# Kernel tuning notes

Measured on AMD Instinct MI355X. Metric: run time of the kernel, lower is better.

Reference implementation:

```python
import jax, jax.numpy as jnp
import numpy as np

T, S, B = 128, 128, 32          # enc len, dec len, batch
H, D = 512, 512                 # hidden == input_size (required by module)
VE, VD = 32000, 32000           # encoder / decoder vocab


def setup_inputs() -> dict:
    key = jax.random.key(0)
    ks = jax.random.split(key, 14)
    s = 0.05  # init scale, mimics uniform(-initrange, initrange)
    n = lambda k, shape: jax.random.normal(k, shape, dtype=jnp.float32) * s
    return {
        "encoder_inputs": jax.random.randint(ks[0], (T, B), 0, VE),
        "decoder_inputs": jax.random.randint(ks[1], (S, B), 0, VD),
        "enc_emb": n(ks[2], (VE, D)),
        "dec_emb": n(ks[3], (VD, D)),
        "enc_Wih": n(ks[4], (4 * H, D)),   # torch LSTM gate order: i,f,g,o
        "enc_Whh": n(ks[5], (4 * H, H)),
        "dec_Wih": n(ks[6], (4 * H, H)),
        "dec_Whh": n(ks[7], (4 * H, H)),
        "attn_enc_W": n(ks[8], (H, H)),
        "attn_enc_b": n(ks[9], (H,)),
        "attn_dec_W": n(ks[10], (H, H)),
        "attn_dec_b": n(ks[11], (H,)),
        "out_W": n(ks[12], (VD, H)),
        "out_b": n(ks[13], (VD,)),
    }


def lstm(x, Wih, Whh, h0, c0):
    """Bias-free LSTM over seq-first x [T,B,Din]; returns (ys [T,B,H], (h,c))."""
    def step(carry, xt):
        h, c = carry
        gates = xt @ Wih.T + h @ Whh.T
        i, f, g, o = jnp.split(gates, 4, axis=-1)
        c = jax.nn.sigmoid(f) * c + jax.nn.sigmoid(i) * jnp.tanh(g)
        h = jax.nn.sigmoid(o) * jnp.tanh(c)
        return (h, c), h
    (h, c), ys = jax.lax.scan(step, (h0, c0), x)
    return ys, (h, c)


def reference(encoder_inputs, decoder_inputs, enc_emb, dec_emb,
              enc_Wih, enc_Whh, dec_Wih, dec_Whh,
              attn_enc_W, attn_enc_b, attn_dec_W, attn_dec_b,
              out_W, out_b):
    Bsz = encoder_inputs.shape[1]
    Hd = enc_Whh.shape[1]
    z = jnp.zeros((Bsz, Hd), dtype=enc_Whh.dtype)
    # encoder
    xe = enc_emb[encoder_inputs]                      # [T,B,D]
    enc_out, (h, c) = lstm(xe, enc_Wih, enc_Whh, z, z)
    # decoder (teacher forcing), init from encoder final state
    xd = dec_emb[decoder_inputs]                      # [S,B,H]
    dec_out, _ = lstm(xd, dec_Wih, dec_Whh, h, c)     # [S,B,H]
    # per-timestep dot attention, vectorized over all decoder steps
    scores = jnp.einsum('tbh,sbh->sbt', enc_out, dec_out)   # [S,B,T]
    attn = jax.nn.softmax(scores, axis=-1)
    ctx = jnp.einsum('sbt,tbh->sbh', attn, enc_out)          # [S,B,H]
    hidden = jnp.tanh(ctx @ attn_enc_W.T + attn_enc_b
                      + dec_out @ attn_dec_W.T + attn_dec_b)
    logits = hidden @ out_W.T + out_b                        # [S,B,VD]
    return jax.nn.log_softmax(logits, axis=-1)
```

## Files before the change

kernel.cpp:

```cpp
#include <hip/hip_runtime.h>
#include <stdint.h>

#define TT 128
#define BB 32
#define HH 512
#define MM 4096
#define VD 32000
#define NLB 16

typedef float f32x4 __attribute__((ext_vector_type(4)));
typedef short s16x8 __attribute__((ext_vector_type(8)));
typedef unsigned long long u64;

#define TAGMASK 0x0001000100010001ull

__device__ __forceinline__ ushort f2bf(float f){
  uint u = __float_as_uint(f);
  return (ushort)((u + 0x7fffu + ((u >> 16) & 1u)) >> 16);
}
__device__ __forceinline__ float bfl(uint v){ return __uint_as_float(v << 16); }
__device__ __forceinline__ float bfh(uint v){ return __uint_as_float(v & 0xffff0000u); }
__device__ __forceinline__ float bfu(ushort v){ return __uint_as_float(((uint)v) << 16); }
__device__ __forceinline__ float fast_tanh(float x){
  return 1.f - 2.f / (1.f + __expf(2.f * x));
}

__global__ void k_init(u64* hbuf){
  int i = blockIdx.x * 256 + threadIdx.x;
  if (i < 4096) hbuf[i] = 0ull;
  else if (i < 8192) hbuf[i] = TAGMASK;
}

__global__ __launch_bounds__(256) void k_cvt(const float* __restrict__ s, ushort* __restrict__ d, int n4){
  int i = blockIdx.x * 256 + threadIdx.x;
  int st = gridDim.x * 256;
  for (; i < n4; i += st){
    f32x4 v = *(const f32x4*)(s + (size_t)i * 4);
    ushort4 o; o.x = f2bf(v[0]); o.y = f2bf(v[1]); o.z = f2bf(v[2]); o.w = f2bf(v[3]);
    *(ushort4*)(d + (size_t)i * 4) = o;
  }
}

__global__ __launch_bounds__(128) void k_embed(const int* __restrict__ ids, const float* __restrict__ emb,
                                               ushort* __restrict__ out){
  int row = blockIdx.x, t = threadIdx.x;
  int id = ids[row];
  f32x4 v = *(const f32x4*)(emb + (size_t)id * HH + t * 4);
  ushort4 o; o.x = f2bf(v[0]); o.y = f2bf(v[1]); o.z = f2bf(v[2]); o.w = f2bf(v[3]);
  *(ushort4*)(out + (size_t)row * HH + t * 4) = o;
}

__global__ __launch_bounds__(128) void k_concatB(const float* __restrict__ We, const float* __restrict__ Wd,
                                                 ushort* __restrict__ Bc){
  int n = blockIdx.x, t = threadIdx.x;
  f32x4 a = *(const f32x4*)(We + (size_t)n * HH + t * 4);
  f32x4 b = *(const f32x4*)(Wd + (size_t)n * HH + t * 4);
  ushort4 oa, ob;
  oa.x = f2bf(a[0]); oa.y = f2bf(a[1]); oa.z = f2bf(a[2]); oa.w = f2bf(a[3]);
  ob.x = f2bf(b[0]); ob.y = f2bf(b[1]); ob.z = f2bf(b[2]); ob.w = f2bf(b[3]);
  *(ushort4*)(Bc + (size_t)n * 1024 + t * 4) = oa;
  *(ushort4*)(Bc + (size_t)n * 1024 + 512 + t * 4) = ob;
}
__global__ void k_bsum(const float* a, const float* b, float* o){
  int i = blockIdx.x * 256 + threadIdx.x;
  if (i < HH) o[i] = a[i] + b[i];
}

template<bool BIAS, bool TANH, bool OUTBF, bool LSE>
__global__ __launch_bounds__(256) void k_gemm(const ushort* __restrict__ A, const ushort* __restrict__ Bm,
                                              const float* __restrict__ bias, void* __restrict__ Cout,
                                              int Mtot, int Ntot, int K,
                                              float* __restrict__ pbufM, float* __restrict__ pbufL){
  __shared__ __align__(16) ushort As[128 * 32];
  __shared__ __align__(16) ushort Bs[128 * 32];
  __shared__ float sMm[2][128], sMl[2][128];
  const int tid = threadIdx.x;
  const int m0 = blockIdx.y << 7, n0 = blockIdx.x << 7;
  const int wid = tid >> 6, lane = tid & 63;
  const int wm = wid >> 1, wn = wid & 1;
  const int lr = lane & 15, lg = lane >> 4;
  const int lk = lg << 3, cr = lg << 2;
  f32x4 acc[4][4];
  for (int i = 0; i < 4; ++i)
    for (int j = 0; j < 4; ++j)
      acc[i][j] = (f32x4){0.f, 0.f, 0.f, 0.f};
  const int c0 = tid, c1 = tid + 256;
  const size_t ar0 = (size_t)(m0 + (c0 >> 2)) * K + ((c0 & 3) << 3);
  const size_t ar1 = (size_t)(m0 + (c1 >> 2)) * K + ((c1 & 3) << 3);
  const size_t br0 = (size_t)(n0 + (c0 >> 2)) * K + ((c0 & 3) << 3);
  const size_t br1 = (size_t)(n0 + (c1 >> 2)) * K + ((c1 & 3) << 3);
  for (int k0 = 0; k0 < K; k0 += 32){
    __syncthreads();
    __builtin_amdgcn_global_load_lds((const __attribute__((address_space(1))) void*)(A + ar0 + k0),
                                     (__attribute__((address_space(3))) void*)(As + (c0 << 3)), 16, 0, 0);
    __builtin_amdgcn_global_load_lds((const __attribute__((address_space(1))) void*)(A + ar1 + k0),
                                     (__attribute__((address_space(3))) void*)(As + (c1 << 3)), 16, 0, 0);
    __builtin_amdgcn_global_load_lds((const __attribute__((address_space(1))) void*)(Bm + br0 + k0),
                                     (__attribute__((address_space(3))) void*)(Bs + (c0 << 3)), 16, 0, 0);
    __builtin_amdgcn_global_load_lds((const __attribute__((address_space(1))) void*)(Bm + br1 + k0),
                                     (__attribute__((address_space(3))) void*)(Bs + (c1 << 3)), 16, 0, 0);
    __syncthreads();
    s16x8 af[4], bf[4];
    #pragma unroll
    for (int f = 0; f < 4; ++f){
      af[f] = *(const s16x8*)(As + ((wm << 6) + (f << 4) + lr) * 32 + lk);
      bf[f] = *(const s16x8*)(Bs + ((wn << 6) + (f << 4) + lr) * 32 + lk);
    }
    #pragma unroll
    for (int fm = 0; fm < 4; ++fm)
      #pragma unroll
      for (int fn = 0; fn < 4; ++fn)
        acc[fm][fn] = __builtin_amdgcn_mfma_f32_16x16x32_bf16(af[fm], bf[fn], acc[fm][fn], 0, 0, 0);
  }
  float bv4[4];
  #pragma unroll
  for (int fn = 0; fn < 4; ++fn)
    bv4[fn] = BIAS ? bias[n0 + (wn << 6) + (fn << 4) + lr] : 0.f;
  float mv[16], lv[16];
  #pragma unroll
  for (int fm = 0; fm < 4; ++fm){
    #pragma unroll
    for (int r = 0; r < 4; ++r){
      const int rw = m0 + (wm << 6) + (fm << 4) + cr + r;
      float vs[4], vmax = -1e30f;
      #pragma unroll
      for (int fn = 0; fn < 4; ++fn){
        float v = acc[fm][fn][r] + bv4[fn];
        if (TANH) v = tanhf(v);
        vs[fn] = v;
        if (LSE) vmax = fmaxf(vmax, v);
        const size_t off = (size_t)rw * Ntot + (n0 + (wn << 6) + (fn << 4) + lr);
        if (OUTBF) ((ushort*)Cout)[off] = f2bf(v);
        else       ((float*)Cout)[off] = v;
      }
      if (LSE){
        float l4 = 0.f;
        #pragma unroll
        for (int fn = 0; fn < 4; ++fn) l4 += __expf(vs[fn] - vmax);
        mv[(fm << 2) + r] = vmax; lv[(fm << 2) + r] = l4;
      }
    }
  }
  if (LSE){
    #pragma unroll
    for (int q = 0; q < 16; ++q){
      #pragma unroll
      for (int off = 1; off < 16; off <<= 1){
        float m2 = __shfl_xor(mv[q], off), l2 = __shfl_xor(lv[q], off);
        float nm = fmaxf(mv[q], m2);
        lv[q] = lv[q] * __expf(mv[q] - nm) + l2 * __expf(m2 - nm);
        mv[q] = nm;
      }
    }
    float selM = -1e30f, selL = 0.f;
    #pragma unroll
    for (int q = 0; q < 16; ++q){
      selM = (lr == q) ? mv[q] : selM;
      selL = (lr == q) ? lv[q] : selL;
    }
    const int lrow = (wm << 6) + ((lr >> 2) << 4) + (lg << 2) + (lr & 3);
    sMm[wn][lrow] = selM; sMl[wn][lrow] = selL;
    __syncthreads();
    if (tid < 128){
      float ma = sMm[0][tid], mb = sMm[1][tid];
      float nm = fmaxf(ma, mb);
      float l = sMl[0][tid] * __expf(ma - nm) + sMl[1][tid] * __expf(mb - nm);
      pbufM[(size_t)(m0 + tid) * 256 + blockIdx.x] = nm;
      pbufL[(size_t)(m0 + tid) * 256 + blockIdx.x] = l;
    }
  }
}

__global__ __launch_bounds__(512) void k_lstm(const float* __restrict__ GinE, const float* __restrict__ GinD,
                                              const float* __restrict__ WhhE, const float* __restrict__ WhhD,
                                              u64* __restrict__ hbuf,
                                              ushort* __restrict__ encO, ushort* __restrict__ decO,
                                              ushort* __restrict__ Ac){
  __shared__ __align__(16) ushort wlds[4 * 32 * 512];
  __shared__ __align__(16) float gbuf[128 * 36];
  const int tid = threadIdx.x;
  const int bk = blockIdx.x;
  const int J0 = bk << 5;
  const int w = tid >> 6, lane = tid & 63;
  const int m = w & 1, g = w >> 1;
  const int lr = lane & 15, lg = lane >> 4;
  const int cb = tid >> 3, cq = tid & 7;

  f32x4 c4 = {0.f, 0.f, 0.f, 0.f};
  f32x4 gin4[4];

  if (tid < 256){
    const float* gp = GinE + (size_t)cb * 2048 + J0 + (cq << 2);
    gin4[0] = *(const f32x4*)(gp);
    gin4[1] = *(const f32x4*)(gp + 512);
    gin4[2] = *(const f32x4*)(gp + 1024);
    gin4[3] = *(const f32x4*)(gp + 1536);
  }

  const char* wr0 = (const char*)wlds + (g << 15) + (lr << 10);
  const int swz = (lr & 7) << 4;

  for (int s = 0; s < 256; ++s){
    const int ph = s >> 7, t = s & 127;
    if (t == 0){
      const float* Whh = ph ? WhhD : WhhE;
      const int rr = tid >> 2, kq = tid & 3;
      const int gg = rr >> 5, jl = rr & 31;
      const float* src = Whh + (size_t)((gg << 9) + J0 + jl) * 512 + (kq << 7);
      char* dstrow = (char*)wlds + (size_t)(((gg << 5) + jl) << 10);
      #pragma unroll
      for (int i = 0; i < 16; ++i){
        f32x4 wa = *(const f32x4*)(src + (i << 3));
        f32x4 wc = *(const f32x4*)(src + (i << 3) + 4);
        uint4 pk;
        pk.x = ((uint)f2bf(wa[1]) << 16) | f2bf(wa[0]);
        pk.y = ((uint)f2bf(wa[3]) << 16) | f2bf(wa[2]);
        pk.z = ((uint)f2bf(wc[1]) << 16) | f2bf(wc[0]);
        pk.w = ((uint)f2bf(wc[3]) << 16) | f2bf(wc[2]);
        *(uint4*)(dstrow + ((((kq << 4) + i) << 4) ^ ((jl & 7) << 4))) = pk;
      }
      __syncthreads();
    }
    const uint pat = ((s >> 1) & 1) ? 0x00010001u : 0u;
    const char* hp = (const char*)hbuf + ((s & 1) << 15) + (m << 14) + (lg << 8) + (lr << 4);
    uint4 vv[16];
    for (;;){
      #pragma unroll
      for (int ks = 0; ks < 16; ++ks)
        asm volatile("global_load_dwordx4 %0, %1, off sc0 sc1"
                     : "=v"(vv[ks]) : "v"(hp + (ks << 10)) : "memory");
      asm volatile("s_waitcnt vmcnt(0)" ::: "memory");
      __builtin_amdgcn_sched_barrier(0);
      uint bad = 0u;
      #pragma unroll
      for (int ks = 0; ks < 16; ++ks)
        bad |= (vv[ks].x ^ pat) | (vv[ks].y ^ pat) | (vv[ks].z ^ pat) | (vv[ks].w ^ pat);
      if (__all((bad & 0x00010001u) == 0u)) break;
    }
    f32x4 a0 = {0.f, 0.f, 0.f, 0.f}, a1 = {0.f, 0.f, 0.f, 0.f};
    #pragma unroll
    for (int ks = 0; ks < 16; ++ks){
      union { uint4 u; s16x8 v; } ua;
      ua.u.x = vv[ks].x & 0xFFFEFFFEu;
      ua.u.y = vv[ks].y & 0xFFFEFFFEu;
      ua.u.z = vv[ks].z & 0xFFFEFFFEu;
      ua.u.w = vv[ks].w & 0xFFFEFFFEu;
      const int ko = ((ks << 6) + (lg << 4)) ^ swz;
      const s16x8 b0 = *(const s16x8*)(wr0 + ko);
      const s16x8 b1 = *(const s16x8*)(wr0 + (16 << 10) + ko);
      a0 = __builtin_amdgcn_mfma_f32_16x16x32_bf16(ua.v, b0, a0, 0, 0, 0);
      a1 = __builtin_amdgcn_mfma_f32_16x16x32_bf16(ua.v, b1, a1, 0, 0, 0);
    }
    #pragma unroll
    for (int r = 0; r < 4; ++r){
      const int row = (g << 5) + (m << 4) + (lg << 2) + r;
      gbuf[row * 36 + lr] = a0[r];
      gbuf[row * 36 + 16 + lr] = a1[r];
    }
    __syncthreads();
    if (tid < 256){
      f32x4 z0 = *(const f32x4*)(gbuf + (      cb) * 36 + (cq << 2));
      f32x4 z1 = *(const f32x4*)(gbuf + (32 + cb) * 36 + (cq << 2));
      f32x4 z2 = *(const f32x4*)(gbuf + (64 + cb) * 36 + (cq << 2));
      f32x4 z3 = *(const f32x4*)(gbuf + (96 + cb) * 36 + (cq << 2));
      z0 += gin4[0]; z1 += gin4[1]; z2 += gin4[2]; z3 += gin4[3];
      const uint tgn = (uint)(((s + 1) >> 1) & 1);
      u64 htag = 0ull, hclean = 0ull;
      #pragma unroll
      for (int e = 0; e < 4; ++e){
        const float si = 1.f / (1.f + __expf(-z0[e]));
        const float sf = 1.f / (1.f + __expf(-z1[e]));
        const float so = 1.f / (1.f + __expf(-z3[e]));
        const float cc = sf * c4[e] + si * fast_tanh(z2[e]);
        c4[e] = cc;
        const uint hb = (uint)f2bf(so * fast_tanh(cc));
        hclean |= (u64)hb << (e << 4);
        htag   |= (u64)((hb & 0xFFFEu) | tgn) << (e << 4);
      }
      __hip_atomic_store(hbuf + (((size_t)((s + 1) & 1)) << 12) + ((cb >> 4) << 11) + (bk << 7)
                              + ((cq >> 1) << 5) + ((cb & 15) << 1) + (cq & 1), htag,
                         __ATOMIC_RELAXED, __HIP_MEMORY_SCOPE_AGENT);
      u64* hallq = (u64*)(ph ? decO : encO);
      __hip_atomic_store(hallq + (size_t)(t * 32 + cb) * 128 + (bk << 3) + cq, hclean,
                         __ATOMIC_RELAXED, __HIP_MEMORY_SCOPE_AGENT);
      if (ph)
        __hip_atomic_store((u64*)Ac + (size_t)(t * 32 + cb) * 256 + 128 + (bk << 3) + cq, hclean,
                           __ATOMIC_RELAXED, __HIP_MEMORY_SCOPE_AGENT);
      if (s < 255){
        const int s2 = s + 1, t2 = s2 & 127;
        const float* G2 = (s2 >> 7) ? GinD : GinE;
        const float* gp = G2 + (size_t)(t2 * 32 + cb) * 2048 + J0 + (cq << 2);
        gin4[0] = *(const f32x4*)(gp);
        gin4[1] = *(const f32x4*)(gp + 512);
        gin4[2] = *(const f32x4*)(gp + 1024);
        gin4[3] = *(const f32x4*)(gp + 1536);
      }
    }
  }
}

__global__ __launch_bounds__(256) void k_attn(const ushort* __restrict__ enc, const ushort* __restrict__ dec,
                                              ushort* __restrict__ Ac){
  __shared__ __align__(16) float dec_lds[16 * 512];
  __shared__ __align__(16) float P[16 * 128];
  const int tid = threadIdx.x;
  const int b = blockIdx.x & 31, st = blockIdx.x >> 5;
  const int s0 = st << 4;
  for (int j = 0; j < 4; ++j){
    int e8 = tid + (j << 8);
    int sl = e8 >> 6, k = (e8 & 63) << 3;
    uint4 v = *(const uint4*)(dec + ((size_t)((s0 + sl) * 32 + b) << 9) + k);
    float* dst = dec_lds + sl * 512 + k;
    dst[0] = bfl(v.x); dst[1] = bfh(v.x); dst[2] = bfl(v.y); dst[3] = bfh(v.y);
    dst[4] = bfl(v.z); dst[5] = bfh(v.z); dst[6] = bfl(v.w); dst[7] = bfh(v.w);
  }
  __syncthreads();
  {
    const int tl = tid & 127, sh = tid >> 7;
    const ushort* erow = enc + ((size_t)(tl * 32 + b) << 9);
    float acc8[8] = {0.f, 0.f, 0.f, 0.f, 0.f, 0.f, 0.f, 0.f};
    for (int k = 0; k < 512; k += 8){
      uint4 v = *(const uint4*)(erow + k);
      const float e0 = bfl(v.x), e1 = bfh(v.x), e2 = bfl(v.y), e3 = bfh(v.y);
      const float e4 = bfl(v.z), e5 = bfh(v.z), e6 = bfl(v.w), e7 = bfh(v.w);
      const float* dl = dec_lds + (sh << 3) * 512 + k;
      #pragma unroll
      for (int i = 0; i < 8; ++i){
        f32x4 d0 = *(const f32x4*)(dl + i * 512);
        f32x4 d1 = *(const f32x4*)(dl + i * 512 + 4);
        acc8[i] += d0[0]*e0 + d0[1]*e1 + d0[2]*e2 + d0[3]*e3
                 + d1[0]*e4 + d1[1]*e5 + d1[2]*e6 + d1[3]*e7;
      }
    }
    #pragma unroll
    for (int i = 0; i < 8; ++i) P[((sh << 3) + i) * 128 + tl] = acc8[i];
  }
  __syncthreads();
  {
    const int r = tid >> 4, i = tid & 15;
    float* prow = P + r * 128 + (i << 3);
    float v[8], mx = -1e30f;
    #pragma unroll
    for (int j = 0; j < 8; ++j){ v[j] = prow[j]; mx = fmaxf(mx, v[j]); }
    #pragma unroll
    for (int off = 1; off < 16; off <<= 1) mx = fmaxf(mx, __shfl_xor(mx, off));
    float l = 0.f;
    #pragma unroll
    for (int j = 0; j < 8; ++j){ v[j] = __expf(v[j] - mx); l += v[j]; }
    #pragma unroll
    for (int off = 1; off < 16; off <<= 1) l += __shfl_xor(l, off);
    const float inv = 1.f / l;
    #pragma unroll
    for (int j = 0; j < 8; ++j) prow[j] = v[j] * inv;
  }
  __syncthreads();
  {
    const int h0 = tid << 1;
    float acc[16][2];
    #pragma unroll
    for (int sl = 0; sl < 16; ++sl){ acc[sl][0] = 0.f; acc[sl][1] = 0.f; }
    const ushort* ecol = enc + ((size_t)b << 9) + h0;
    for (int t = 0; t < 128; ++t){
      uint v = *(const uint*)(ecol + (size_t)t * 16384);
      const float e0 = bfl(v), e1 = bfh(v);
      #pragma unroll
      for (int sl = 0; sl < 16; ++sl){
        const float p = P[sl * 128 + t];
        acc[sl][0] += p * e0; acc[sl][1] += p * e1;
      }
    }
    #pragma unroll
    for (int sl = 0; sl < 16; ++sl){
      const int mm = (s0 + sl) * 32 + b;
      uint u = ((uint)f2bf(acc[sl][1]) << 16) | (uint)f2bf(acc[sl][0]);
      *(uint*)(Ac + (size_t)mm * 1024 + h0) = u;
    }
  }
}

__global__ __launch_bounds__(256) void k_lse2(const float* __restrict__ pM, const float* __restrict__ pL,
                                              float* __restrict__ lse){
  const int row = (blockIdx.x << 2) + (threadIdx.x >> 6);
  const int lane = threadIdx.x & 63;
  float m = -1e30f, l = 0.f;
  for (int i = lane; i < 250; i += 64){
    float m2 = pM[(size_t)row * 256 + i], l2 = pL[(size_t)row * 256 + i];
    float nm = fmaxf(m, m2);
    l = l * __expf(m - nm) + l2 * __expf(m2 - nm);
    m = nm;
  }
  #pragma unroll
  for (int off = 32; off; off >>= 1){
    float m2 = __shfl_xor(m, off), l2 = __shfl_xor(l, off);
    float nm = fmaxf(m, m2);
    l = l * __expf(m - nm) + l2 * __expf(m2 - nm);
    m = nm;
  }
  if (lane == 0) lse[row] = m + __logf(l);
}

__global__ __launch_bounds__(256) void k_sub(float* __restrict__ out, const float* __restrict__ lse){
  const int row = blockIdx.x;
  const float s = lse[row];
  float* p = out + (size_t)row * VD;
  for (int i4 = threadIdx.x; i4 < VD / 4; i4 += 256){
    f32x4 v = *(const f32x4*)(p + ((size_t)i4 << 2));
    v[0] -= s; v[1] -= s; v[2] -= s; v[3] -= s;
    *(f32x4*)(p + ((size_t)i4 << 2)) = v;
  }
}

extern "C" void kernel_launch(void* const* d_in, const int* in_sizes, int n_in,
                              void* d_out, int out_size, void* d_ws, size_t ws_size,
                              hipStream_t stream){
  const int*   enc_in  = (const int*)d_in[0];
  const int*   dec_in  = (const int*)d_in[1];
  const float* enc_emb = (const float*)d_in[2];
  const float* dec_emb = (const float*)d_in[3];
  const float* WihE    = (const float*)d_in[4];
  const float* WhhE    = (const float*)d_in[5];
  const float* WihD    = (const float*)d_in[6];
  const float* WhhD    = (const float*)d_in[7];
  const float* We      = (const float*)d_in[8];
  const float* be      = (const float*)d_in[9];
  const float* Wd      = (const float*)d_in[10];
  const float* bd      = (const float*)d_in[11];
  const float* outW    = (const float*)d_in[12];
  const float* outb    = (const float*)d_in[13];
  float* out = (float*)d_out;

  char* ws = (char*)d_ws;
  size_t off = 0;
  auto alloc = [&](size_t bytes){ void* p = ws + off; off += (bytes + 255) & ~(size_t)255; return p; };
  ushort* xe    = (ushort*)alloc((size_t)MM * HH * 2);
  ushort* xd    = (ushort*)alloc((size_t)MM * HH * 2);
  ushort* WihEb = (ushort*)alloc((size_t)2048 * 512 * 2);
  ushort* WihDb = (ushort*)alloc((size_t)2048 * 512 * 2);
  ushort* Bc    = (ushort*)alloc((size_t)512 * 1024 * 2);
  float*  bsum  = (float*)alloc(512 * 4);
  ushort* outWb = (ushort*)alloc((size_t)VD * HH * 2);
  ushort* encO  = (ushort*)alloc((size_t)MM * HH * 2);
  ushort* decO  = (ushort*)alloc((size_t)MM * HH * 2);
  u64*    hbuf  = (u64*)alloc(8192 * 8);
  ushort* Ac    = (ushort*)alloc((size_t)MM * 1024 * 2);
  ushort* hid   = (ushort*)alloc((size_t)MM * HH * 2);
  float*  lse   = (float*)alloc(MM * 4);
  float*  pbufM = (float*)alloc((size_t)MM * 256 * 4);
  float*  pbufL = (float*)alloc((size_t)MM * 256 * 4);
  float* GinE = out;
  float* GinD = out + (size_t)MM * 2048;

  k_init<<<dim3(32), dim3(256), 0, stream>>>(hbuf);
  k_cvt<<<dim3(1024), dim3(256), 0, stream>>>(WihE, WihEb, 2048 * 512 / 4);
  k_cvt<<<dim3(1024), dim3(256), 0, stream>>>(WihD, WihDb, 2048 * 512 / 4);
  k_cvt<<<dim3(2048), dim3(256), 0, stream>>>(outW, outWb, VD * HH / 4);
  k_concatB<<<dim3(512), dim3(128), 0, stream>>>(We, Wd, Bc);
  k_bsum<<<dim3(2), dim3(256), 0, stream>>>(be, bd, bsum);
  k_embed<<<dim3(MM), dim3(128), 0, stream>>>(enc_in, enc_emb, xe);
  k_embed<<<dim3(MM), dim3(128), 0, stream>>>(dec_in, dec_emb, xd);
  k_gemm<false, false, false, false><<<dim3(16, 32), dim3(256), 0, stream>>>(xe, WihEb, (const float*)nullptr, GinE, MM, 2048, 512, nullptr, nullptr);
  k_gemm<false, false, false, false><<<dim3(16, 32), dim3(256), 0, stream>>>(xd, WihDb, (const float*)nullptr, GinD, MM, 2048, 512, nullptr, nullptr);
  k_lstm<<<dim3(NLB), dim3(512), 0, stream>>>(GinE, GinD, WhhE, WhhD, hbuf, encO, decO, Ac);
  k_attn<<<dim3(256), dim3(256), 0, stream>>>(encO, decO, Ac);
  k_gemm<true, true, true, false><<<dim3(4, 32), dim3(256), 0, stream>>>(Ac, Bc, bsum, hid, MM, 512, 1024, nullptr, nullptr);
  k_gemm<true, false, false, true><<<dim3(250, 32), dim3(256), 0, stream>>>(hid, outWb, outb, out, MM, VD, 512, pbufM, pbufL);
  k_lse2<<<dim3(1024), dim3(256), 0, stream>>>(pbufM, pbufL, lse);
  k_sub<<<dim3(MM), dim3(256), 0, stream>>>(out, lse);
}
```

Measured before the change: 1.664 ms.

## Restructure LSTM step: in-register gate exchange, single-wave h polling, fuse LSE into subtract

The persistent LSTM kernel now redistributes MFMA gate outputs across lanes with ds_bpermute, so every thread computes two hidden units directly. This removes the LDS gate buffer round trip and the half-idle elementwise phase. Polling for the next hidden state is moved to the end of the step and done by two waves only, which stage the unpacked h into LDS for the next step's MFMA, cutting redundant global polling. The separate LSE reduction kernel is folded into the subtract kernel, removing one launch and the lse buffer. In exchange, each step issues many bpermutes and every block recomputes its row's reduction.

```diff
diff --git a/kernel.cpp b/kernel.cpp
--- a/kernel.cpp
+++ b/kernel.cpp
@@ -9,6 +9,7 @@
 #define NLB 16
 
 typedef float f32x4 __attribute__((ext_vector_type(4)));
+typedef float f32x2 __attribute__((ext_vector_type(2)));
 typedef short s16x8 __attribute__((ext_vector_type(8)));
 typedef unsigned long long u64;
 
@@ -20,10 +21,10 @@
 }
 __device__ __forceinline__ float bfl(uint v){ return __uint_as_float(v << 16); }
 __device__ __forceinline__ float bfh(uint v){ return __uint_as_float(v & 0xffff0000u); }
-__device__ __forceinline__ float bfu(ushort v){ return __uint_as_float(((uint)v) << 16); }
 __device__ __forceinline__ float fast_tanh(float x){
   return 1.f - 2.f / (1.f + __expf(2.f * x));
 }
+__device__ __forceinline__ float sigm(float x){ return 1.f / (1.f + __expf(-x)); }
 
 __global__ void k_init(u64* hbuf){
   int i = blockIdx.x * 256 + threadIdx.x;
@@ -177,125 +178,137 @@
                                               ushort* __restrict__ encO, ushort* __restrict__ decO,
                                               ushort* __restrict__ Ac){
   __shared__ __align__(16) ushort wlds[4 * 32 * 512];
-  __shared__ __align__(16) float gbuf[128 * 36];
+  __shared__ __align__(16) uint4 abuf[2048];
   const int tid = threadIdx.x;
   const int bk = blockIdx.x;
   const int J0 = bk << 5;
   const int w = tid >> 6, lane = tid & 63;
-  const int m = w & 1, g = w >> 1;
+  const int m = w & 1, jt = w >> 1;
   const int lr = lane & 15, lg = lane >> 4;
-  const int cb = tid >> 3, cq = tid & 7;
-
-  f32x4 c4 = {0.f, 0.f, 0.f, 0.f};
-  f32x4 gin4[4];
-
-  if (tid < 256){
-    const float* gp = GinE + (size_t)cb * 2048 + J0 + (cq << 2);
-    gin4[0] = *(const f32x4*)(gp);
-    gin4[1] = *(const f32x4*)(gp + 512);
-    gin4[2] = *(const f32x4*)(gp + 1024);
-    gin4[3] = *(const f32x4*)(gp + 1536);
-  }
-
-  const char* wr0 = (const char*)wlds + (g << 15) + (lr << 10);
+  const int beta = lane >> 2, p = lane & 3, myr = beta & 3;
+  const int b_own = (m << 4) + beta;
+  const int j_own = J0 + (jt << 3) + (p << 1);
+
+  float cc0 = 0.f, cc1 = 0.f;
+  const int sgb = (lane & 48) + ((lane & 3) << 1);
+  const int ad_l0 = sgb << 2, ad_l1 = (sgb + 1) << 2;
+  const int ad_h0 = (sgb + 8) << 2, ad_h1 = (sgb + 9) << 2;
+  const char* wrow0 = (const char*)wlds + ((((lr >> 3) << 5) + (jt << 3) + (lr & 7)) << 10);
+  const char* wrow1 = wrow0 + (64 << 10);
   const int swz = (lr & 7) << 4;
+
+  auto stageW = [&](const float* Whh){
+    const int rr = tid >> 2, kq = tid & 3;
+    const int gg = rr >> 5, jl = rr & 31;
+    const float* src = Whh + (size_t)((gg << 9) + J0 + jl) * 512 + (kq << 7);
+    char* dstrow = (char*)wlds + (size_t)(((gg << 5) + jl) << 10);
+    #pragma unroll
+    for (int i = 0; i < 16; ++i){
+      f32x4 wa = *(const f32x4*)(src + (i << 3));
+      f32x4 wc = *(const f32x4*)(src + (i << 3) + 4);
+      uint4 pk;
+      pk.x = ((uint)f2bf(wa[1]) << 16) | f2bf(wa[0]);
+      pk.y = ((uint)f2bf(wa[3]) << 16) | f2bf(wa[2]);
+      pk.z = ((uint)f2bf(wc[1]) << 16) | f2bf(wc[0]);
+      pk.w = ((uint)f2bf(wc[3]) << 16) | f2bf(wc[2]);
+      *(uint4*)(dstrow + ((((kq << 4) + i) << 4) ^ ((jl & 7) << 4))) = pk;
+    }
+  };
+
+  float gi0, gi1, gf0, gf1, gg0, gg1, go0, go1;
+  f32x2 nxi, nxf, nxg, nxo;
+  {
+    const float* gp = GinE + (size_t)b_own * 2048 + j_own;
+    nxi = *(const f32x2*)(gp);        nxf = *(const f32x2*)(gp + 512);
+    nxg = *(const f32x2*)(gp + 1024); nxo = *(const f32x2*)(gp + 1536);
+  }
+  stageW(WhhE);
+  { uint4 z = {0u, 0u, 0u, 0u};
+    #pragma unroll
+    for (int i = 0; i < 4; ++i) abuf[(tid << 2) + i] = z; }
+  __syncthreads();
 
   for (int s = 0; s < 256; ++s){
     const int ph = s >> 7, t = s & 127;
-    if (t == 0){
-      const float* Whh = ph ? WhhD : WhhE;
-      const int rr = tid >> 2, kq = tid & 3;
-      const int gg = rr >> 5, jl = rr & 31;
-      const float* src = Whh + (size_t)((gg << 9) + J0 + jl) * 512 + (kq << 7);
-      char* dstrow = (char*)wlds + (size_t)(((gg << 5) + jl) << 10);
-      #pragma unroll
-      for (int i = 0; i < 16; ++i){
-        f32x4 wa = *(const f32x4*)(src + (i << 3));
-        f32x4 wc = *(const f32x4*)(src + (i << 3) + 4);
-        uint4 pk;
-        pk.x = ((uint)f2bf(wa[1]) << 16) | f2bf(wa[0]);
-        pk.y = ((uint)f2bf(wa[3]) << 16) | f2bf(wa[2]);
-        pk.z = ((uint)f2bf(wc[1]) << 16) | f2bf(wc[0]);
-        pk.w = ((uint)f2bf(wc[3]) << 16) | f2bf(wc[2]);
-        *(uint4*)(dstrow + ((((kq << 4) + i) << 4) ^ ((jl & 7) << 4))) = pk;
-      }
-      __syncthreads();
-    }
-    const uint pat = ((s >> 1) & 1) ? 0x00010001u : 0u;
-    const char* hp = (const char*)hbuf + ((s & 1) << 15) + (m << 14) + (lg << 8) + (lr << 4);
-    uint4 vv[16];
-    for (;;){
-      #pragma unroll
-      for (int ks = 0; ks < 16; ++ks)
-        asm volatile("global_load_dwordx4 %0, %1, off sc0 sc1"
-                     : "=v"(vv[ks]) : "v"(hp + (ks << 10)) : "memory");
-      asm volatile("s_waitcnt vmcnt(0)" ::: "memory");
-      __builtin_amdgcn_sched_barrier(0);
-      uint bad = 0u;
-      #pragma unroll
-      for (int ks = 0; ks < 16; ++ks)
-        bad |= (vv[ks].x ^ pat) | (vv[ks].y ^ pat) | (vv[ks].z ^ pat) | (vv[ks].w ^ pat);
-      if (__all((bad & 0x00010001u) == 0u)) break;
+    if (s == 128){ stageW(WhhD); __syncthreads(); }
+    gi0 = nxi[0]; gi1 = nxi[1]; gf0 = nxf[0]; gf1 = nxf[1];
+    gg0 = nxg[0]; gg1 = nxg[1]; go0 = nxo[0]; go1 = nxo[1];
+    if (s < 255){
+      const int s2 = s + 1, t2 = s2 & 127;
+      const float* G2 = (s2 >> 7) ? GinD : GinE;
+      const float* gp = G2 + (size_t)((t2 << 5) + b_own) * 2048 + j_own;
+      nxi = *(const f32x2*)(gp);        nxf = *(const f32x2*)(gp + 512);
+      nxg = *(const f32x2*)(gp + 1024); nxo = *(const f32x2*)(gp + 1536);
     }
     f32x4 a0 = {0.f, 0.f, 0.f, 0.f}, a1 = {0.f, 0.f, 0.f, 0.f};
     #pragma unroll
     for (int ks = 0; ks < 16; ++ks){
       union { uint4 u; s16x8 v; } ua;
-      ua.u.x = vv[ks].x & 0xFFFEFFFEu;
-      ua.u.y = vv[ks].y & 0xFFFEFFFEu;
-      ua.u.z = vv[ks].z & 0xFFFEFFFEu;
-      ua.u.w = vv[ks].w & 0xFFFEFFFEu;
+      ua.u = abuf[(m << 10) + (ks << 6) + (lg << 4) + lr];
       const int ko = ((ks << 6) + (lg << 4)) ^ swz;
-      const s16x8 b0 = *(const s16x8*)(wr0 + ko);
-      const s16x8 b1 = *(const s16x8*)(wr0 + (16 << 10) + ko);
+      const s16x8 b0 = *(const s16x8*)(wrow0 + ko);
+      const s16x8 b1 = *(const s16x8*)(wrow1 + ko);
       a0 = __builtin_amdgcn_mfma_f32_16x16x32_bf16(ua.v, b0, a0, 0, 0, 0);
       a1 = __builtin_amdgcn_mfma_f32_16x16x32_bf16(ua.v, b1, a1, 0, 0, 0);
     }
+    float vi0 = 0.f, vi1 = 0.f, vf0 = 0.f, vf1 = 0.f, vg0 = 0.f, vg1 = 0.f, vo0 = 0.f, vo1 = 0.f;
     #pragma unroll
     for (int r = 0; r < 4; ++r){
-      const int row = (g << 5) + (m << 4) + (lg << 2) + r;
-      gbuf[row * 36 + lr] = a0[r];
-      gbuf[row * 36 + 16 + lr] = a1[r];
+      const int ti0 = __builtin_amdgcn_ds_bpermute(ad_l0, __float_as_int(a0[r]));
+      const int ti1 = __builtin_amdgcn_ds_bpermute(ad_l1, __float_as_int(a0[r]));
+      const int tf0 = __builtin_amdgcn_ds_bpermute(ad_h0, __float_as_int(a0[r]));
+      const int tf1 = __builtin_amdgcn_ds_bpermute(ad_h1, __float_as_int(a0[r]));
+      const int tg0 = __builtin_amdgcn_ds_bpermute(ad_l0, __float_as_int(a1[r]));
+      const int tg1 = __builtin_amdgcn_ds_bpermute(ad_l1, __float_as_int(a1[r]));
+      const int to0 = __builtin_amdgcn_ds_bpermute(ad_h0, __float_as_int(a1[r]));
+      const int to1 = __builtin_amdgcn_ds_bpermute(ad_h1, __float_as_int(a1[r]));
+      if (myr == r){
+        vi0 = __int_as_float(ti0); vi1 = __int_as_float(ti1);
+        vf0 = __int_as_float(tf0); vf1 = __int_as_float(tf1);
+        vg0 = __int_as_float(tg0); vg1 = __int_as_float(tg1);
+        vo0 = __int_as_float(to0); vo1 = __int_as_float(to1);
+      }
+    }
+    const uint tgn = (uint)(((s + 1) >> 1) & 1);
+    float h0f, h1f;
+    { const float si = sigm(vi0 + gi0), sf = sigm(vf0 + gf0), so = sigm(vo0 + go0);
+      cc0 = sf * cc0 + si * fast_tanh(vg0 + gg0); h0f = so * fast_tanh(cc0); }
+    { const float si = sigm(vi1 + gi1), sf = sigm(vf1 + gf1), so = sigm(vo1 + go1);
+      cc1 = sf * cc1 + si * fast_tanh(vg1 + gg1); h1f = so * fast_tanh(cc1); }
+    const uint hb0 = (uint)f2bf(h0f), hb1 = (uint)f2bf(h1f);
+    const uint hclean = (hb1 << 16) | hb0;
+    const uint htag = (((hb1 & 0xFFFEu) | tgn) << 16) | ((hb0 & 0xFFFEu) | tgn);
+    __hip_atomic_store((uint*)hbuf + (((s + 1) & 1) << 13) + (m << 12) + (bk << 8) + (jt << 6) + (beta << 2) + p,
+                       htag, __ATOMIC_RELAXED, __HIP_MEMORY_SCOPE_AGENT);
+    uint* hall = (uint*)(ph ? decO : encO);
+    hall[((size_t)((t << 5) + b_own) << 8) + (j_own >> 1)] = hclean;
+    if (ph) ((uint*)Ac)[((size_t)((t << 5) + b_own) << 9) + 256 + (j_own >> 1)] = hclean;
+    if (w >= 6 && s < 255){
+      const uint pat = (((s + 1) >> 1) & 1) ? 0x00010001u : 0u;
+      const char* hp = (const char*)hbuf + (((s + 1) & 1) << 15) + (m << 14) + (lg << 8) + (lr << 4);
+      uint4 vv[16];
+      for (;;){
+        #pragma unroll
+        for (int ks = 0; ks < 16; ++ks)
+          asm volatile("global_load_dwordx4 %0, %1, off sc0 sc1"
+                       : "=v"(vv[ks]) : "v"(hp + (ks << 10)) : "memory");
+        asm volatile("s_waitcnt vmcnt(0)" ::: "memory");
+        __builtin_amdgcn_sched_barrier(0);
+        uint bad = 0u;
+        #pragma unroll
+        for (int ks = 0; ks < 16; ++ks)
+          bad |= (vv[ks].x ^ pat) | (vv[ks].y ^ pat) | (vv[ks].z ^ pat) | (vv[ks].w ^ pat);
+        if (__all((bad & 0x00010001u) == 0u)) break;
+      }
+      char* ab = (char*)abuf + (m << 14) + (lg << 8) + (lr << 4);
+      #pragma unroll
+      for (int ks = 0; ks < 16; ++ks){
+        vv[ks].x &= 0xFFFEFFFEu; vv[ks].y &= 0xFFFEFFFEu;
+        vv[ks].z &= 0xFFFEFFFEu; vv[ks].w &= 0xFFFEFFFEu;
+        *(uint4*)(ab + (ks << 10)) = vv[ks];
+      }
     }
     __syncthreads();
-    if (tid < 256){
-      f32x4 z0 = *(const f32x4*)(gbuf + (      cb) * 36 + (cq << 2));
-      f32x4 z1 = *(const f32x4*)(gbuf + (32 + cb) * 36 + (cq << 2));
-      f32x4 z2 = *(const f32x4*)(gbuf + (64 + cb) * 36 + (cq << 2));
-      f32x4 z3 = *(const f32x4*)(gbuf + (96 + cb) * 36 + (cq << 2));
-      z0 += gin4[0]; z1 += gin4[1]; z2 += gin4[2]; z3 += gin4[3];
-      const uint tgn = (uint)(((s + 1) >> 1) & 1);
-      u64 htag = 0ull, hclean = 0ull;
-      #pragma unroll
-      for (int e = 0; e < 4; ++e){
-        const float si = 1.f / (1.f + __expf(-z0[e]));
-        const float sf = 1.f / (1.f + __expf(-z1[e]));
-        const float so = 1.f / (1.f + __expf(-z3[e]));
-        const float cc = sf * c4[e] + si * fast_tanh(z2[e]);
-        c4[e] = cc;
-        const uint hb = (uint)f2bf(so * fast_tanh(cc));
-        hclean |= (u64)hb << (e << 4);
-        htag   |= (u64)((hb & 0xFFFEu) | tgn) << (e << 4);
-      }
-      __hip_atomic_store(hbuf + (((size_t)((s + 1) & 1)) << 12) + ((cb >> 4) << 11) + (bk << 7)
-                              + ((cq >> 1) << 5) + ((cb & 15) << 1) + (cq & 1), htag,
-                         __ATOMIC_RELAXED, __HIP_MEMORY_SCOPE_AGENT);
-      u64* hallq = (u64*)(ph ? decO : encO);
-      __hip_atomic_store(hallq + (size_t)(t * 32 + cb) * 128 + (bk << 3) + cq, hclean,
-                         __ATOMIC_RELAXED, __HIP_MEMORY_SCOPE_AGENT);
-      if (ph)
-        __hip_atomic_store((u64*)Ac + (size_t)(t * 32 + cb) * 256 + 128 + (bk << 3) + cq, hclean,
-                           __ATOMIC_RELAXED, __HIP_MEMORY_SCOPE_AGENT);
-      if (s < 255){
-        const int s2 = s + 1, t2 = s2 & 127;
-        const float* G2 = (s2 >> 7) ? GinD : GinE;
-        const float* gp = G2 + (size_t)(t2 * 32 + cb) * 2048 + J0 + (cq << 2);
-        gin4[0] = *(const f32x4*)(gp);
-        gin4[1] = *(const f32x4*)(gp + 512);
-        gin4[2] = *(const f32x4*)(gp + 1024);
-        gin4[3] = *(const f32x4*)(gp + 1536);
-      }
-    }
   }
 }
 
@@ -378,32 +391,32 @@
   }
 }
 
-__global__ __launch_bounds__(256) void k_lse2(const float* __restrict__ pM, const float* __restrict__ pL,
-                                              float* __restrict__ lse){
-  const int row = (blockIdx.x << 2) + (threadIdx.x >> 6);
-  const int lane = threadIdx.x & 63;
-  float m = -1e30f, l = 0.f;
-  for (int i = lane; i < 250; i += 64){
-    float m2 = pM[(size_t)row * 256 + i], l2 = pL[(size_t)row * 256 + i];
-    float nm = fmaxf(m, m2);
-    l = l * __expf(m - nm) + l2 * __expf(m2 - nm);
-    m = nm;
-  }
-  #pragma unroll
-  for (int off = 32; off; off >>= 1){
-    float m2 = __shfl_xor(m, off), l2 = __shfl_xor(l, off);
-    float nm = fmaxf(m, m2);
-    l = l * __expf(m - nm) + l2 * __expf(m2 - nm);
-    m = nm;
-  }
-  if (lane == 0) lse[row] = m + __logf(l);
-}
-
-__global__ __launch_bounds__(256) void k_sub(float* __restrict__ out, const float* __restrict__ lse){
+__global__ __launch_bounds__(256) void k_sub(float* __restrict__ out,
+                                             const float* __restrict__ pM, const float* __restrict__ pL){
+  __shared__ float slse;
   const int row = blockIdx.x;
-  const float s = lse[row];
+  const int tid = threadIdx.x;
+  if (tid < 64){
+    float m = -1e30f, l = 0.f;
+    for (int i = tid; i < 250; i += 64){
+      float m2 = pM[(size_t)row * 256 + i], l2 = pL[(size_t)row * 256 + i];
+      float nm = fmaxf(m, m2);
+      l = l * __expf(m - nm) + l2 * __expf(m2 - nm);
+      m = nm;
+    }
+    #pragma unroll
+    for (int off = 32; off; off >>= 1){
+      float m2 = __shfl_xor(m, off), l2 = __shfl_xor(l, off);
+      float nm = fmaxf(m, m2);
+      l = l * __expf(m - nm) + l2 * __expf(m2 - nm);
+      m = nm;
+    }
+    if (tid == 0) slse = m + __logf(l);
+  }
+  __syncthreads();
+  const float s = slse;
   float* p = out + (size_t)row * VD;
-  for (int i4 = threadIdx.x; i4 < VD / 4; i4 += 256){
+  for (int i4 = tid; i4 < VD / 4; i4 += 256){
     f32x4 v = *(const f32x4*)(p + ((size_t)i4 << 2));
     v[0] -= s; v[1] -= s; v[2] -= s; v[3] -= s;
     *(f32x4*)(p + ((size_t)i4 << 2)) = v;
@@ -444,7 +457,6 @@
   u64*    hbuf  = (u64*)alloc(8192 * 8);
   ushort* Ac    = (ushort*)alloc((size_t)MM * 1024 * 2);
   ushort* hid   = (ushort*)alloc((size_t)MM * HH * 2);
-  float*  lse   = (float*)alloc(MM * 4);
   float*  pbufM = (float*)alloc((size_t)MM * 256 * 4);
   float*  pbufL = (float*)alloc((size_t)MM * 256 * 4);
   float* GinE = out;
@@ -464,6 +476,5 @@
   k_attn<<<dim3(256), dim3(256), 0, stream>>>(encO, decO, Ac);
   k_gemm<true, true, true, false><<<dim3(4, 32), dim3(256), 0, stream>>>(Ac, Bc, bsum, hid, MM, 512, 1024, nullptr, nullptr);
   k_gemm<true, false, false, true><<<dim3(250, 32), dim3(256), 0, stream>>>(hid, outWb, outb, out, MM, VD, 512, pbufM, pbufL);
-  k_lse2<<<dim3(1024), dim3(256), 0, stream>>>(pbufM, pbufL, lse);
-  k_sub<<<dim3(MM), dim3(256), 0, stream>>>(out, lse);
-}
+  k_sub<<<dim3(MM), dim3(256), 0, stream>>>(out, pbufM, pbufL);
+}
```

After: 1.709 ms. 1.03x slower.

## Store logits as bf16 in-place and fuse LSE reduction into final subtract kernel

Applied to the files above, without the earlier changes.

The vocab GEMM now writes bf16 logits into the upper half of each fp32 output row (leading dimension 64000 ushorts), halving its store traffic. The separate lse reduction kernel is folded into k_sub, which stages the bf16 row in shared memory, reduces the partial max/sum, then expands to fp32 minus lse over the same row. This removes one launch and about half of the logits write/read bandwidth, at the cost of bf16 rounding of the logits before log-softmax and a row-aliasing scheme that depends on each block fully reading its row before writing it.

```diff
diff --git a/kernel.cpp b/kernel.cpp
--- a/kernel.cpp
+++ b/kernel.cpp
@@ -69,7 +69,7 @@
 template<bool BIAS, bool TANH, bool OUTBF, bool LSE>
 __global__ __launch_bounds__(256) void k_gemm(const ushort* __restrict__ A, const ushort* __restrict__ Bm,
                                               const float* __restrict__ bias, void* __restrict__ Cout,
-                                              int Mtot, int Ntot, int K,
+                                              int Mtot, int Ntot, int K, int ldc,
                                               float* __restrict__ pbufM, float* __restrict__ pbufL){
   __shared__ __align__(16) ushort As[128 * 32];
   __shared__ __align__(16) ushort Bs[128 * 32];
@@ -129,7 +129,7 @@
         if (TANH) v = tanhf(v);
         vs[fn] = v;
         if (LSE) vmax = fmaxf(vmax, v);
-        const size_t off = (size_t)rw * Ntot + (n0 + (wn << 6) + (fn << 4) + lr);
+        const size_t off = (size_t)rw * ldc + (n0 + (wn << 6) + (fn << 4) + lr);
         if (OUTBF) ((ushort*)Cout)[off] = f2bf(v);
         else       ((float*)Cout)[off] = v;
       }
@@ -378,35 +378,42 @@
   }
 }
 
-__global__ __launch_bounds__(256) void k_lse2(const float* __restrict__ pM, const float* __restrict__ pL,
-                                              float* __restrict__ lse){
-  const int row = (blockIdx.x << 2) + (threadIdx.x >> 6);
-  const int lane = threadIdx.x & 63;
-  float m = -1e30f, l = 0.f;
-  for (int i = lane; i < 250; i += 64){
-    float m2 = pM[(size_t)row * 256 + i], l2 = pL[(size_t)row * 256 + i];
-    float nm = fmaxf(m, m2);
-    l = l * __expf(m - nm) + l2 * __expf(m2 - nm);
-    m = nm;
-  }
-  #pragma unroll
-  for (int off = 32; off; off >>= 1){
-    float m2 = __shfl_xor(m, off), l2 = __shfl_xor(l, off);
-    float nm = fmaxf(m, m2);
-    l = l * __expf(m - nm) + l2 * __expf(m2 - nm);
-    m = nm;
-  }
-  if (lane == 0) lse[row] = m + __logf(l);
-}
-
-__global__ __launch_bounds__(256) void k_sub(float* __restrict__ out, const float* __restrict__ lse){
+__global__ __launch_bounds__(256) void k_sub(float* __restrict__ out,
+                                             const float* __restrict__ pM, const float* __restrict__ pL){
+  __shared__ float slse;
+  __shared__ __align__(16) ushort rowb[VD];
   const int row = blockIdx.x;
-  const float s = lse[row];
+  const int tid = threadIdx.x;
+  const ushort* src = (const ushort*)out + (size_t)row * 64000 + 32000;
+  for (int i = tid; i < VD / 8; i += 256)
+    *(uint4*)(rowb + (i << 3)) = *(const uint4*)(src + (i << 3));
+  if (tid < 64){
+    float m = -1e30f, l = 0.f;
+    for (int i = tid; i < 250; i += 64){
+      float m2 = pM[(size_t)row * 256 + i], l2 = pL[(size_t)row * 256 + i];
+      float nm = fmaxf(m, m2);
+      l = l * __expf(m - nm) + l2 * __expf(m2 - nm);
+      m = nm;
+    }
+    #pragma unroll
+    for (int off = 32; off; off >>= 1){
+      float m2 = __shfl_xor(m, off), l2 = __shfl_xor(l, off);
+      float nm = fmaxf(m, m2);
+      l = l * __expf(m - nm) + l2 * __expf(m2 - nm);
+      m = nm;
+    }
+    if (tid == 0) slse = m + __logf(l);
+  }
+  __syncthreads();
+  const float s = slse;
   float* p = out + (size_t)row * VD;
-  for (int i4 = threadIdx.x; i4 < VD / 4; i4 += 256){
-    f32x4 v = *(const f32x4*)(p + ((size_t)i4 << 2));
-    v[0] -= s; v[1] -= s; v[2] -= s; v[3] -= s;
-    *(f32x4*)(p + ((size_t)i4 << 2)) = v;
+  for (int i = tid; i < VD / 8; i += 256){
+    uint4 v = *(const uint4*)(rowb + (i << 3));
+    f32x4 o0, o1;
+    o0[0] = bfl(v.x) - s; o0[1] = bfh(v.x) - s; o0[2] = bfl(v.y) - s; o0[3] = bfh(v.y) - s;
+    o1[0] = bfl(v.z) - s; o1[1] = bfh(v.z) - s; o1[2] = bfl(v.w) - s; o1[3] = bfh(v.w) - s;
+    *(f32x4*)(p + (i << 3)) = o0;
+    *(f32x4*)(p + (i << 3) + 4) = o1;
   }
 }
 
@@ -444,11 +451,11 @@
   u64*    hbuf  = (u64*)alloc(8192 * 8);
   ushort* Ac    = (ushort*)alloc((size_t)MM * 1024 * 2);
   ushort* hid   = (ushort*)alloc((size_t)MM * HH * 2);
-  float*  lse   = (float*)alloc(MM * 4);
   float*  pbufM = (float*)alloc((size_t)MM * 256 * 4);
   float*  pbufL = (float*)alloc((size_t)MM * 256 * 4);
   float* GinE = out;
   float* GinD = out + (size_t)MM * 2048;
+  ushort* logb = (ushort*)out + 32000;
 
   k_init<<<dim3(32), dim3(256), 0, stream>>>(hbuf);
   k_cvt<<<dim3(1024), dim3(256), 0, stream>>>(WihE, WihEb, 2048 * 512 / 4);
@@ -458,12 +465,11 @@
   k_bsum<<<dim3(2), dim3(256), 0, stream>>>(be, bd, bsum);
   k_embed<<<dim3(MM), dim3(128), 0, stream>>>(enc_in, enc_emb, xe);
   k_embed<<<dim3(MM), dim3(128), 0, stream>>>(dec_in, dec_emb, xd);
-  k_gemm<false, false, false, false><<<dim3(16, 32), dim3(256), 0, stream>>>(xe, WihEb, (const float*)nullptr, GinE, MM, 2048, 512, nullptr, nullptr);
-  k_gemm<false, false, false, false><<<dim3(16, 32), dim3(256), 0, stream>>>(xd, WihDb, (const float*)nullptr, GinD, MM, 2048, 512, nullptr, nullptr);
+  k_gemm<false, false, false, false><<<dim3(16, 32), dim3(256), 0, stream>>>(xe, WihEb, (const float*)nullptr, GinE, MM, 2048, 512, 2048, nullptr, nullptr);
+  k_gemm<false, false, false, false><<<dim3(16, 32), dim3(256), 0, stream>>>(xd, WihDb, (const float*)nullptr, GinD, MM, 2048, 512, 2048, nullptr, nullptr);
   k_lstm<<<dim3(NLB), dim3(512), 0, stream>>>(GinE, GinD, WhhE, WhhD, hbuf, encO, decO, Ac);
   k_attn<<<dim3(256), dim3(256), 0, stream>>>(encO, decO, Ac);
-  k_gemm<true, true, true, false><<<dim3(4, 32), dim3(256), 0, stream>>>(Ac, Bc, bsum, hid, MM, 512, 1024, nullptr, nullptr);
-  k_gemm<true, false, false, true><<<dim3(250, 32), dim3(256), 0, stream>>>(hid, outWb, outb, out, MM, VD, 512, pbufM, pbufL);
-  k_lse2<<<dim3(1024), dim3(256), 0, stream>>>(pbufM, pbufL, lse);
-  k_sub<<<dim3(MM), dim3(256), 0, stream>>>(out, lse);
-}
+  k_gemm<true, true, true, false><<<dim3(4, 32), dim3(256), 0, stream>>>(Ac, Bc, bsum, hid, MM, 512, 1024, 512, nullptr, nullptr);
+  k_gemm<true, false, true, true><<<dim3(250, 32), dim3(256), 0, stream>>>(hid, outWb, outb, logb, MM, VD, 512, 64000, pbufM, pbufL);
+  k_sub<<<dim3(MM), dim3(256), 0, stream>>>(out, pbufM, pbufL);
+}
```

Measured after the change: 1.643 ms. Within noise of the previous version (-1.3%).
